# Kernel tuning notes

Hardware: AMD Instinct MI355X
Metric: run time of the kernel (lower is better)

## Reference

```python
import jax, jax.numpy as jnp
import numpy as np

N_NODES = 50000
N_EDGES = 1600000
D = 128  # input_dim == hidden_dim


def glorot(key, shape):
    lim = float(np.sqrt(6.0 / (shape[0] + shape[1])))
    return jax.random.uniform(key, shape, jnp.float32, -lim, lim)


def setup_inputs() -> dict:
    key = jax.random.key(0)
    ks = jax.random.split(key, 10)
    x = jax.random.normal(ks[0], (N_NODES, D), jnp.float32)
    edge_index = jax.random.randint(ks[1], (2, N_EDGES), 0, N_NODES, jnp.int64)
    edge_attr = jax.random.normal(ks[2], (N_EDGES, D), jnp.float32)
    # SAGEConv params per layer: lin_l (W,b), lin_r (W, no bias)
    W1l = glorot(ks[3], (D, D)); b1l = jnp.zeros((D,), jnp.float32)
    W1r = glorot(ks[4], (D, D))
    W2l = glorot(ks[5], (D, D)); b2l = jnp.zeros((D,), jnp.float32)
    W2r = glorot(ks[6], (D, D))
    return {"x": x, "edge_index": edge_index, "edge_attr": edge_attr,
            "W1l": W1l, "b1l": b1l, "W1r": W1r,
            "W2l": W2l, "b2l": b2l, "W2r": W2r}


def sage_layer(z, src, dst, edge_attr, Wl, bl, Wr):
    # message: gather x_j, add edge_attr, relu  -> [E, D]
    msg = jax.nn.relu(z[src] + edge_attr)
    # mean aggregation at destination nodes
    agg = jax.ops.segment_sum(msg, dst, num_segments=N_NODES)
    cnt = jax.ops.segment_sum(jnp.ones((dst.shape[0], 1), z.dtype), dst,
                              num_segments=N_NODES)
    agg = agg / jnp.maximum(cnt, 1.0)
    # lin_l(agg) + lin_r(x) (root weight, no bias on lin_r)
    return agg @ Wl + bl + z @ Wr


def reference(x, edge_index, edge_attr, W1l, b1l, W1r, W2l, b2l, W2r):
    src, dst = edge_index[0], edge_index[1]
    z = sage_layer(x, src, dst, edge_attr, W1l, b1l, W1r)
    z = jax.nn.relu(z)  # activation between layers; dropout=0, normalize='none'
    z = sage_layer(z, src, dst, edge_attr, W2l, b2l, W2r)
    return z
```

## Files before the change

### kernel.cpp

```cpp
#include <hip/hip_runtime.h>

#define D 128

typedef __attribute__((ext_vector_type(8))) short bf16x8;
typedef __attribute__((ext_vector_type(4))) float f32x4;

__device__ inline unsigned short f2bf(float f) {
    union { float f; unsigned u; } v; v.f = f;
    unsigned r = v.u + 0x7FFF + ((v.u >> 16) & 1);
    return (unsigned short)(r >> 16);
}
__device__ inline float bf2f(unsigned short h) {
    union { unsigned u; float f; } v; v.u = ((unsigned)h) << 16; return v.f;
}


__global__ __launch_bounds__(256) void castx_kernel(const float* __restrict__ x,
                                                    unsigned short* __restrict__ xb, int n4) {
    int i = blockIdx.x * 256 + threadIdx.x;
    if (i < n4) {
        float4 v = reinterpret_cast<const float4*>(x)[i];
        ushort4 r;
        r.x = f2bf(v.x); r.y = f2bf(v.y); r.z = f2bf(v.z); r.w = f2bf(v.w);
        reinterpret_cast<ushort4*>(xb)[i] = r;
    }
}

__global__ __launch_bounds__(256) void wcast_kernel(const float* __restrict__ W1l,
                                                    const float* __restrict__ W1r,
                                                    const float* __restrict__ W2l,
                                                    const float* __restrict__ W2r,
                                                    unsigned short* __restrict__ Wt1,
                                                    unsigned short* __restrict__ Wt2) {
    int c = blockIdx.x, k = threadIdx.x;
    float v1 = (k < 128) ? W1l[k * 128 + c] : W1r[(k - 128) * 128 + c];
    float v2 = (k < 128) ? W2l[k * 128 + c] : W2r[(k - 128) * 128 + c];
    Wt1[c * 256 + k] = f2bf(v1);
    Wt2[c * 256 + k] = f2bf(v2);
}


__global__ __launch_bounds__(256) void count_kernel(const int* __restrict__ dst,
                                                    int* __restrict__ cnt, int E) {
    int e = blockIdx.x * 256 + threadIdx.x;
    if (e < E) atomicAdd(&cnt[dst[e]], 1);
}

__global__ __launch_bounds__(256) void psum_kernel(const int* __restrict__ cnt,
                                                   int* __restrict__ bsum, int n) {
    __shared__ int wsh[4];
    int b = blockIdx.x, tid = threadIdx.x;
    int i0 = b * 1024 + tid * 4;
    int s = 0;
    #pragma unroll
    for (int j = 0; j < 4; ++j) { int i = i0 + j; if (i < n) s += cnt[i]; }
    #pragma unroll
    for (int d = 1; d < 64; d <<= 1) s += __shfl_xor(s, d, 64);
    if ((tid & 63) == 0) wsh[tid >> 6] = s;
    __syncthreads();
    if (tid == 0) bsum[b] = wsh[0] + wsh[1] + wsh[2] + wsh[3];
}

__global__ __launch_bounds__(64) void bscan_kernel(const int* __restrict__ bsum,
                                                   int* __restrict__ bpre, int nb) {
    int t = threadIdx.x;
    int v = (t < nb) ? bsum[t] : 0;
    int sc = v;
    #pragma unroll
    for (int d = 1; d < 64; d <<= 1) { int u = __shfl_up(sc, d, 64); if (t >= d) sc += u; }
    if (t < nb) bpre[t] = sc - v;
}

__global__ __launch_bounds__(256) void fscan_kernel(const int* __restrict__ cnt,
                                                    const int* __restrict__ bpre,
                                                    int* __restrict__ off,
                                                    int* __restrict__ cursor, int n) {
    __shared__ int wsum[4];
    int b = blockIdx.x, tid = threadIdx.x;
    int lane = tid & 63, wv = tid >> 6;
    int i0 = b * 1024 + tid * 4;
    int v[4]; int s = 0;
    #pragma unroll
    for (int j = 0; j < 4; ++j) { int i = i0 + j; v[j] = (i < n) ? cnt[i] : 0; s += v[j]; }
    int sc = s;
    #pragma unroll
    for (int d = 1; d < 64; d <<= 1) { int u = __shfl_up(sc, d, 64); if (lane >= d) sc += u; }
    if (lane == 63) wsum[wv] = sc;
    __syncthreads();
    int wp = 0;
    for (int j = 0; j < wv; ++j) wp += wsum[j];
    int base = bpre[b] + wp + sc - s;
    #pragma unroll
    for (int j = 0; j < 4; ++j) {
        int i = i0 + j;
        if (i < n) { cursor[i] = base; off[i + 1] = base + v[j]; }
        base += v[j];
    }
    if (b == 0 && tid == 0) off[0] = 0;
}

__global__ __launch_bounds__(256) void fill_kernel(const int* __restrict__ src,
                                                   const int* __restrict__ dst,
                                                   int* __restrict__ cursor,
                                                   int2* __restrict__ pairs, int E) {
    int e = blockIdx.x * 256 + threadIdx.x;
    if (e < E) {
        int d = dst[e];
        int slot = atomicAdd(&cursor[d], 1);
        pairs[slot] = make_int2(src[e], e);
    }
}


__global__ __launch_bounds__(64) void aggregate_kernel(const unsigned short* __restrict__ featb,
                                                       const float* __restrict__ ea,
                                                       const int* __restrict__ off,
                                                       const int2* __restrict__ pairs,
                                                       unsigned short* __restrict__ aggb) {
    int nd = blockIdx.x;
    int t = threadIdx.x;
    int half = t >> 5, l32 = t & 31;
    int s = off[nd], e = off[nd + 1];
    float a0 = 0.f, a1 = 0.f, a2 = 0.f, a3 = 0.f;
    for (int p = s + half; p < e; p += 2) {
        int2 pr = pairs[p];
        const float4 ev = *reinterpret_cast<const float4*>(&ea[(size_t)pr.y * D + l32 * 4]);
        const ushort4 xv = *reinterpret_cast<const ushort4*>(&featb[(size_t)pr.x * D + l32 * 4]);
        a0 += fmaxf(bf2f(xv.x) + ev.x, 0.f);
        a1 += fmaxf(bf2f(xv.y) + ev.y, 0.f);
        a2 += fmaxf(bf2f(xv.z) + ev.z, 0.f);
        a3 += fmaxf(bf2f(xv.w) + ev.w, 0.f);
    }
    a0 += __shfl_xor(a0, 32, 64);
    a1 += __shfl_xor(a1, 32, 64);
    a2 += __shfl_xor(a2, 32, 64);
    a3 += __shfl_xor(a3, 32, 64);
    int deg = e - s;
    float inv = 1.f / (float)(deg > 0 ? deg : 1);
    if (t < 32) {
        ushort4 r;
        r.x = f2bf(a0 * inv); r.y = f2bf(a1 * inv);
        r.z = f2bf(a2 * inv); r.w = f2bf(a3 * inv);
        *reinterpret_cast<ushort4*>(&aggb[(size_t)nd * D + l32 * 4]) = r;
    }
}


template <int RELU, int OUT_BF16>
__global__ __launch_bounds__(256) void gemm_mfma_kernel(const unsigned short* __restrict__ A1,
                                                        const unsigned short* __restrict__ A2,
                                                        const unsigned short* __restrict__ Wt,
                                                        const float* __restrict__ bias,
                                                        float* __restrict__ outf,
                                                        unsigned short* __restrict__ outb,
                                                        int MT) {
    int tid = threadIdx.x;
    int w = tid >> 6;
    int l = tid & 63;
    int lr = l & 15;
    int lg = l >> 4;
    int c0 = w * 32;

    bf16x8 bfr[2][8];
    #pragma unroll
    for (int t = 0; t < 2; ++t)
        #pragma unroll
        for (int kc = 0; kc < 8; ++kc)
            bfr[t][kc] = *reinterpret_cast<const bf16x8*>(
                &Wt[(size_t)(c0 + t * 16 + lr) * 256 + kc * 32 + lg * 8]);

    for (int mt = blockIdx.x; mt < MT; mt += gridDim.x) {
        int r0 = mt * 16;
        f32x4 acc0 = {0.f, 0.f, 0.f, 0.f};
        f32x4 acc1 = {0.f, 0.f, 0.f, 0.f};
        #pragma unroll
        for (int kc = 0; kc < 8; ++kc) {
            const unsigned short* Ap = (kc < 4) ? A1 : A2;
            int k = (kc & 3) * 32 + lg * 8;
            bf16x8 af = *reinterpret_cast<const bf16x8*>(&Ap[(size_t)(r0 + lr) * D + k]);
            acc0 = __builtin_amdgcn_mfma_f32_16x16x32_bf16(af, bfr[0][kc], acc0, 0, 0, 0);
            acc1 = __builtin_amdgcn_mfma_f32_16x16x32_bf16(af, bfr[1][kc], acc1, 0, 0, 0);
        }
        #pragma unroll
        for (int t = 0; t < 2; ++t) {
            const f32x4& a = t ? acc1 : acc0;
            int col = c0 + t * 16 + lr;
            float bv = bias[col];
            #pragma unroll
            for (int r = 0; r < 4; ++r) {
                int row = r0 + lg * 4 + r;
                float v = a[r] + bv;
                if (RELU) v = fmaxf(v, 0.f);
                if (OUT_BF16) outb[(size_t)row * D + col] = f2bf(v);
                else outf[(size_t)row * D + col] = v;
            }
        }
    }
}

extern "C" void kernel_launch(void* const* d_in, const int* in_sizes, int n_in,
                              void* d_out, int out_size, void* d_ws, size_t ws_size,
                              hipStream_t stream) {
    const float* x   = (const float*)d_in[0];
    const int*   ei  = (const int*)d_in[1];
    const float* ea  = (const float*)d_in[2];
    const float* W1l = (const float*)d_in[3];
    const float* b1l = (const float*)d_in[4];
    const float* W1r = (const float*)d_in[5];
    const float* W2l = (const float*)d_in[6];
    const float* b2l = (const float*)d_in[7];
    const float* W2r = (const float*)d_in[8];
    float* out = (float*)d_out;

    const int N = in_sizes[0] / D;
    const int E = in_sizes[1] / 2;
    const int* src = ei;
    const int* dst = ei + E;

    char* ws = (char*)d_ws;
    size_t o = 0;
    auto alloc = [&](size_t bytes) -> void* {
        void* p = ws + o;
        o = (o + bytes + 255) & ~(size_t)255;
        return p;
    };
    int*   cnt    = (int*)alloc((size_t)N * 4);
    int*   off    = (int*)alloc((size_t)(N + 1) * 4);
    int*   cursor = (int*)alloc((size_t)N * 4);
    int*   bsum   = (int*)alloc(256 * 4);
    int*   bpre   = (int*)alloc(256 * 4);
    int2*  pairs  = (int2*)alloc((size_t)E * 8);
    unsigned short* xb   = (unsigned short*)alloc((size_t)N * D * 2);
    unsigned short* z1b  = (unsigned short*)alloc((size_t)N * D * 2);
    unsigned short* aggb = (unsigned short*)alloc((size_t)N * D * 2);
    unsigned short* Wt1  = (unsigned short*)alloc(128 * 256 * 2);
    unsigned short* Wt2  = (unsigned short*)alloc(128 * 256 * 2);
    (void)ws_size; (void)n_in; (void)out_size;

    const int MT = N / 16;
    const int NB = (N + 1023) / 1024;

    castx_kernel<<<(N * D / 4 + 255) / 256, 256, 0, stream>>>(x, xb, N * D / 4);
    wcast_kernel<<<128, 256, 0, stream>>>(W1l, W1r, W2l, W2r, Wt1, Wt2);

    hipMemsetAsync(cnt, 0, (size_t)N * 4, stream);
    count_kernel<<<(E + 255) / 256, 256, 0, stream>>>(dst, cnt, E);
    psum_kernel<<<NB, 256, 0, stream>>>(cnt, bsum, N);
    bscan_kernel<<<1, 64, 0, stream>>>(bsum, bpre, NB);
    fscan_kernel<<<NB, 256, 0, stream>>>(cnt, bpre, off, cursor, N);
    fill_kernel<<<(E + 255) / 256, 256, 0, stream>>>(src, dst, cursor, pairs, E);

    aggregate_kernel<<<N, 64, 0, stream>>>(xb, ea, off, pairs, aggb);
    gemm_mfma_kernel<1, 1><<<1024, 256, 0, stream>>>(aggb, xb, Wt1, b1l, nullptr, z1b, MT);

    aggregate_kernel<<<N, 64, 0, stream>>>(z1b, ea, off, pairs, aggb);
    gemm_mfma_kernel<0, 0><<<1024, 256, 0, stream>>>(aggb, z1b, Wt2, b2l, out, nullptr, MT);
}
```

Measured before the change: 651.7 us.

## Batch edge-pair loads with wave shuffles and unroll aggregate gathers

The aggregation kernel now packs four nodes per 256-thread block, one wavefront per node. Each lane loads one (src, edge) pair per 64-edge chunk and the indices are broadcast with shuffles, replacing the per-iteration pair loads. The gather loop is unrolled to keep two edge fetches per half-wave in flight, and the edge_attr and pair reads use nontemporal loads. This targets index-load latency and block-launch overhead in a gather-bound kernel, at the cost of extra shuffle instructions and more complex tail handling.

```diff
diff --git a/kernel.cpp b/kernel.cpp
--- a/kernel.cpp
+++ b/kernel.cpp
@@ -112,32 +112,67 @@
 }
 
 
-__global__ __launch_bounds__(64) void aggregate_kernel(const unsigned short* __restrict__ featb,
-                                                       const float* __restrict__ ea,
-                                                       const int* __restrict__ off,
-                                                       const int2* __restrict__ pairs,
-                                                       unsigned short* __restrict__ aggb) {
-    int nd = blockIdx.x;
-    int t = threadIdx.x;
+__global__ __launch_bounds__(256) void aggregate_kernel(const unsigned short* __restrict__ featb,
+                                                        const float* __restrict__ ea,
+                                                        const int* __restrict__ off,
+                                                        const long long* __restrict__ pairs,
+                                                        unsigned short* __restrict__ aggb,
+                                                        int N) {
+    int nd = blockIdx.x * 4 + (threadIdx.x >> 6);
+    if (nd >= N) return;
+    int t = threadIdx.x & 63;
     int half = t >> 5, l32 = t & 31;
     int s = off[nd], e = off[nd + 1];
     float a0 = 0.f, a1 = 0.f, a2 = 0.f, a3 = 0.f;
-    for (int p = s + half; p < e; p += 2) {
-        int2 pr = pairs[p];
-        const float4 ev = *reinterpret_cast<const float4*>(&ea[(size_t)pr.y * D + l32 * 4]);
-        const ushort4 xv = *reinterpret_cast<const ushort4*>(&featb[(size_t)pr.x * D + l32 * 4]);
-        a0 += fmaxf(bf2f(xv.x) + ev.x, 0.f);
-        a1 += fmaxf(bf2f(xv.y) + ev.y, 0.f);
-        a2 += fmaxf(bf2f(xv.z) + ev.z, 0.f);
-        a3 += fmaxf(bf2f(xv.w) + ev.w, 0.f);
-    }
+
+    for (int b = s; b < e; b += 64) {
+        int cnt = min(64, e - b);
+        long long prl = (b + t < e) ? __builtin_nontemporal_load(&pairs[b + t]) : 0LL;
+        int psrc = (int)(prl & 0xFFFFFFFFLL);
+        int peid = (int)((unsigned long long)prl >> 32);
+
+        auto fetch = [&](int idx, float4& ev, ushort4& xv) {
+            int sidx = __shfl(psrc, idx, 64);
+            int eidx = __shfl(peid, idx, 64);
+            const float* ep = &ea[(size_t)eidx * D + l32 * 4];
+            ev = make_float4(__builtin_nontemporal_load(ep + 0),
+                             __builtin_nontemporal_load(ep + 1),
+                             __builtin_nontemporal_load(ep + 2),
+                             __builtin_nontemporal_load(ep + 3));
+            xv = *reinterpret_cast<const ushort4*>(&featb[(size_t)sidx * D + l32 * 4]);
+        };
+        auto accum = [&](const float4& ev, const ushort4& xv) {
+            a0 += fmaxf(bf2f(xv.x) + ev.x, 0.f);
+            a1 += fmaxf(bf2f(xv.y) + ev.y, 0.f);
+            a2 += fmaxf(bf2f(xv.z) + ev.z, 0.f);
+            a3 += fmaxf(bf2f(xv.w) + ev.w, 0.f);
+        };
+
+        int p = 0;
+        for (; p + 4 <= cnt; p += 4) {
+            float4 e0; ushort4 x0; fetch(p + half, e0, x0);
+            float4 e1; ushort4 x1; fetch(p + 2 + half, e1, x1);
+            accum(e0, x0);
+            accum(e1, x1);
+        }
+        if (p + 2 <= cnt) {
+            float4 e0; ushort4 x0; fetch(p + half, e0, x0);
+            accum(e0, x0);
+            p += 2;
+        }
+        if (p < cnt) {
+            float4 e0; ushort4 x0; fetch(p, e0, x0);
+            if (half == 0) accum(e0, x0);
+        }
+    }
+
     a0 += __shfl_xor(a0, 32, 64);
     a1 += __shfl_xor(a1, 32, 64);
     a2 += __shfl_xor(a2, 32, 64);
     a3 += __shfl_xor(a3, 32, 64);
     int deg = e - s;
     float inv = 1.f / (float)(deg > 0 ? deg : 1);
-    if (t < 32) {
+    if (half == 0) {
         ushort4 r;
         r.x = f2bf(a0 * inv); r.y = f2bf(a1 * inv);
         r.z = f2bf(a2 * inv); r.w = f2bf(a3 * inv);
@@ -239,20 +274,21 @@
 
     const int MT = N / 16;
     const int NB = (N + 1023) / 1024;
+    const int AGB = (N + 3) / 4;
 
     castx_kernel<<<(N * D / 4 + 255) / 256, 256, 0, stream>>>(x, xb, N * D / 4);
     wcast_kernel<<<128, 256, 0, stream>>>(W1l, W1r, W2l, W2r, Wt1, Wt2);
 
-    hipMemsetAsync(cnt, 0, (size_t)N * 4, stream);
+    (void)hipMemsetAsync(cnt, 0, (size_t)N * 4, stream);
     count_kernel<<<(E + 255) / 256, 256, 0, stream>>>(dst, cnt, E);
     psum_kernel<<<NB, 256, 0, stream>>>(cnt, bsum, N);
     bscan_kernel<<<1, 64, 0, stream>>>(bsum, bpre, NB);
     fscan_kernel<<<NB, 256, 0, stream>>>(cnt, bpre, off, cursor, N);
     fill_kernel<<<(E + 255) / 256, 256, 0, stream>>>(src, dst, cursor, pairs, E);
 
-    aggregate_kernel<<<N, 64, 0, stream>>>(xb, ea, off, pairs, aggb);
+    aggregate_kernel<<<AGB, 256, 0, stream>>>(xb, ea, off, (const long long*)pairs, aggb, N);
     gemm_mfma_kernel<1, 1><<<1024, 256, 0, stream>>>(aggb, xb, Wt1, b1l, nullptr, z1b, MT);
 
-    aggregate_kernel<<<N, 64, 0, stream>>>(z1b, ea, off, pairs, aggb);
+    aggregate_kernel<<<AGB, 256, 0, stream>>>(z1b, ea, off, (const long long*)pairs, aggb, N);
     gemm_mfma_kernel<0, 0><<<1024, 256, 0, stream>>>(aggb, z1b, Wt2, b2l, out, nullptr, MT);
 }
```

Result: faster. 603.7 us (-7.4%).
